# Performance work log

Measured on AMD Instinct MI355X. Metric: run time of the kernel, lower is better.

## Reference

```python
import jax, jax.numpy as jnp
import numpy as np

B, CIN, H, W = 32, 192, 56, 56
COUT, K, PAD, STRIDE = 192, 3, 1, 1


def setup_inputs() -> dict:
    key = jax.random.key(0)
    k1, k2 = jax.random.split(key, 2)
    x = jax.random.normal(k1, (B, CIN, H, W), dtype=jnp.float32)
    # torch Linear: weight [out_feature, in_feature*k*k], bias [out_feature]
    weight = jax.random.normal(k2, (COUT, CIN * K * K), dtype=jnp.float32) * 0.02
    bias = jnp.zeros((COUT,), dtype=jnp.float32)
    return {"x": x, "weight": weight, "bias": bias}


def reference(x, weight, bias):
    # pad H/W with zeros (F.pad constant)
    xp = jnp.pad(x, ((0, 0), (0, 0), (PAD, PAD), (PAD, PAD)))
    Bn, C, Hp, Wp = xp.shape
    Ho = (Hp - K) // STRIDE + 1
    Wo = (Wp - K) // STRIDE + 1
    # im2col matching torch.nn.Unfold layout: feature index = c*K*K + i*K + j
    # small fixed loop over K*K kernel offsets (9 slices), fully vectorized over B,C,Ho,Wo
    patches = jnp.stack(
        [xp[:, :, i : i + Ho * STRIDE : STRIDE, j : j + Wo * STRIDE : STRIDE]
         for i in range(K) for j in range(K)],
        axis=2,
    )  # [B, C, K*K, Ho, Wo]
    cols = patches.reshape(Bn, C * K * K, Ho * Wo)  # [B, C*K*K, L]
    # Linear over transposed unfold: out[b, l, o] = cols[b, :, l] @ weight[o, :].T + bias
    out = jnp.einsum('bkl,ok->bol', cols, weight) + bias[None, :, None]
    # rearrange 'b (h w) c -> b c h w' with h=w=sqrt(L)
    return out.reshape(Bn, COUT, Ho, Wo)
```

## Files before the change

### kernel.cpp

```cpp
#include <hip/hip_runtime.h>

typedef __attribute__((ext_vector_type(8))) short short8;
typedef __attribute__((ext_vector_type(4))) float floatx4;

#define CIN    192
#define COUTN  192
#define HWDIM  56
#define HWSZ   (56*56)
#define KWT    1728
#define TH     4
#define HY     6
#define PH     58
#define CK     32
#define NCHUNK 6
#define MT     64

#define XPACK_SHORTS (32u*6u*58u*58u*32u)
#define WPACK_SHORTS (3u*6u*9u*64u*32u)
#define WS_NEEDED    ((size_t)(XPACK_SHORTS + WPACK_SHORTS) * 2u)

__device__ __forceinline__ short f2bf(float f) {
    union { float f; unsigned u; } v; v.f = f;
    unsigned u = v.u + 0x7FFFu + ((v.u >> 16) & 1u);
    return (short)(u >> 16);
}

__global__ __launch_bounds__(256)
void pack_x(const float* __restrict__ x, short* __restrict__ xp) {
    int idx = blockIdx.x * 256 + threadIdx.x;
    const int TOT = 32 * 6 * 58 * 58 * 4;
    if (idx >= TOT) return;
    int cg  = idx & 3;
    int pix = idx >> 2;
    int xq  = pix % 58;
    int t   = pix / 58;
    int hq  = t % 58;
    int bc  = t / 58;
    int cc  = bc % 6;
    int b   = bc / 6;
    short8 v;
    if (hq == 0 || hq == 57 || xq == 0 || xq == 57) {
        v = (short8){0, 0, 0, 0, 0, 0, 0, 0};
    } else {
        const float* src = x + ((size_t)(b * CIN + cc * 32 + cg * 8) * HWDIM + (hq - 1)) * HWDIM + (xq - 1);
#pragma unroll
        for (int k = 0; k < 8; ++k) v[k] = f2bf(src[(size_t)k * HWSZ]);
    }
    *(short8*)(xp + (size_t)idx * 8) = v;
}

__global__ __launch_bounds__(256)
void pack_w(const float* __restrict__ w, short* __restrict__ wp) {
    int idx = blockIdx.x * 256 + threadIdx.x;
    const int TOT = 3 * 6 * 9 * 64 * 4;
    if (idx >= TOT) return;
    int cg = idx & 3;
    int m  = (idx >> 2) & 63;
    int t  = idx >> 8;
    int off = t % 9;  t /= 9;
    int cc  = t % 6;
    int og  = t / 6;
    short8 v;
#pragma unroll
    for (int k = 0; k < 8; ++k)
        v[k] = f2bf(w[(size_t)(og * 64 + m) * KWT + (cc * 32 + cg * 8 + k) * 9 + off]);
    *(short8*)(wp + (size_t)idx * 8) = v;
}

__global__ __launch_bounds__(256, 2)
void conv_main(const short* __restrict__ xp, const short* __restrict__ wp,
               const float* __restrict__ bias, float* __restrict__ out) {
    __shared__ __align__(16) short sh[HY * PH * CK];

    const int tid  = threadIdx.x;
    const int gh0  = blockIdx.x * TH;
    const int og   = blockIdx.y;
    const int bb   = blockIdx.z;
    const int lane = tid & 63;
    const int wave = tid >> 6;
    const int wm   = wave >> 1;
    const int wn   = wave & 1;
    const int g    = lane >> 4;
    const int col  = lane & 15;

    int ly[7], lx[7];
#pragma unroll
    for (int nt = 0; nt < 7; ++nt) {
        int l = wn * 112 + nt * 16 + col;
        ly[nt] = l / 56;
        lx[nt] = l % 56;
    }

    floatx4 acc[2][7];
#pragma unroll
    for (int mt = 0; mt < 2; ++mt)
#pragma unroll
        for (int nt = 0; nt < 7; ++nt)
            acc[mt][nt] = (floatx4){0.f, 0.f, 0.f, 0.f};

    const short8* wpk = (const short8*)wp;
    const int wlbase = wave * 64;

    for (int cc = 0; cc < NCHUNK; ++cc) {
        if (cc) __syncthreads();

        const short* src = xp + ((size_t)(bb * 6 + cc) * (PH * PH) + (size_t)gh0 * PH) * CK;
#pragma unroll
        for (int j = 0; j < 6; ++j) {
            int idx = j * 256 + tid;
            if (idx < HY * PH * 4) {
                __builtin_amdgcn_global_load_lds(
                    (const __attribute__((address_space(1))) void*)(src + (size_t)idx * 8),
                    (__attribute__((address_space(3))) void*)(sh + (j * 256 + wlbase) * 8),
                    16, 0, 0);
            }
        }

        short8 afr[9][2];
#pragma unroll
        for (int off = 0; off < 9; ++off)
#pragma unroll
            for (int mt = 0; mt < 2; ++mt)
                afr[off][mt] = wpk[((og * 6 + cc) * 9 + off) * 256 + (wm * 32 + mt * 16 + col) * 4 + g];

        __syncthreads();

#pragma unroll
        for (int off = 0; off < 9; ++off) {
            const int di = off / 3, dj = off % 3;
#pragma unroll
            for (int nt = 0; nt < 7; ++nt) {
                short8 bfr = *(const short8*)&sh[((ly[nt] + di) * PH + lx[nt] + dj) * CK + g * 8];
                acc[0][nt] = __builtin_amdgcn_mfma_f32_16x16x32_bf16(afr[off][0], bfr, acc[0][nt], 0, 0, 0);
                acc[1][nt] = __builtin_amdgcn_mfma_f32_16x16x32_bf16(afr[off][1], bfr, acc[1][nt], 0, 0, 0);
            }
        }
    }

#pragma unroll
    for (int mt = 0; mt < 2; ++mt) {
        int o = og * 64 + wm * 32 + mt * 16 + g * 4;
#pragma unroll
        for (int nt = 0; nt < 7; ++nt) {
            int l  = wn * 112 + nt * 16 + col;
            int h  = gh0 + l / 56;
            int ww = l % 56;
            size_t base = ((size_t)(bb * COUTN + o) * HWDIM + h) * HWDIM + ww;
            floatx4 v = acc[mt][nt];
#pragma unroll
            for (int r2 = 0; r2 < 4; ++r2)
                out[base + (size_t)r2 * HWSZ] = v[r2] + bias[o + r2];
        }
    }
}

__global__ __launch_bounds__(256, 2)
void conv3x3_fb(const float* __restrict__ x, const float* __restrict__ w,
                const float* __restrict__ bias, float* __restrict__ out) {
    __shared__ __align__(16) short sh_halo[HY * PH * CK];
    __shared__ __align__(16) short sh_w[9 * MT * CK];
    const int tid = threadIdx.x;
    const int gh0 = blockIdx.x * TH;
    const int o0  = blockIdx.y * MT;
    const int bb  = blockIdx.z;
    const int lane = tid & 63, wave = tid >> 6;
    const int wm = wave >> 1, wn = wave & 1;
    const int g = lane >> 4, col = lane & 15;
    int ly[7], lx[7];
#pragma unroll
    for (int nt = 0; nt < 7; ++nt) {
        int l = wn * 112 + nt * 16 + col;
        ly[nt] = l / 56; lx[nt] = l % 56;
    }
    floatx4 acc[2][7];
#pragma unroll
    for (int mt = 0; mt < 2; ++mt)
#pragma unroll
        for (int nt = 0; nt < 7; ++nt) acc[mt][nt] = (floatx4){0.f,0.f,0.f,0.f};
    for (int cc = 0; cc < NCHUNK; ++cc) {
        const int c0 = cc * CK;
        if (cc) __syncthreads();
        for (int i = tid; i < 4 * HY * PH; i += 256) {
            int xx = i % PH, r = i / PH, y = r % HY, cg = r / HY;
            int gh = gh0 + y - 1, gw = xx - 1;
            bool ok = ((unsigned)gh < 56u) & ((unsigned)gw < 56u);
            const float* src = x + ((size_t)(bb * CIN + c0 + cg * 8) * HWDIM + gh) * HWDIM + gw;
            short8 v;
#pragma unroll
            for (int k = 0; k < 8; ++k) v[k] = f2bf(ok ? src[k * HWSZ] : 0.f);
            *(short8*)&sh_halo[(y * PH + xx) * CK + ((cg ^ ((xx >> 1) & 3)) << 3)] = v;
        }
        for (int i = tid; i < 9 * MT * 4; i += 256) {
            int cg = i & 3, off = (i >> 2) % 9, m = i / 36;
            const float* src = w + (size_t)(o0 + m) * KWT + (c0 + cg * 8) * 9 + off;
            short8 v;
#pragma unroll
            for (int k = 0; k < 8; ++k) v[k] = f2bf(src[k * 9]);
            *(short8*)&sh_w[(off * MT + m) * CK + ((cg ^ ((m >> 1) & 3)) << 3)] = v;
        }
        __syncthreads();
#pragma unroll
        for (int off = 0; off < 9; ++off) {
            const int di = off / 3, dj = off % 3;
            short8 a[2];
#pragma unroll
            for (int mt = 0; mt < 2; ++mt) {
                int m = wm * 32 + mt * 16 + col;
                a[mt] = *(const short8*)&sh_w[(off * MT + m) * CK + ((g ^ ((m >> 1) & 3)) << 3)];
            }
#pragma unroll
            for (int nt = 0; nt < 7; ++nt) {
                int yy = ly[nt] + di, xpp = lx[nt] + dj;
                short8 bfr = *(const short8*)&sh_halo[(yy * PH + xpp) * CK + ((g ^ ((xpp >> 1) & 3)) << 3)];
                acc[0][nt] = __builtin_amdgcn_mfma_f32_16x16x32_bf16(a[0], bfr, acc[0][nt], 0, 0, 0);
                acc[1][nt] = __builtin_amdgcn_mfma_f32_16x16x32_bf16(a[1], bfr, acc[1][nt], 0, 0, 0);
            }
        }
    }
#pragma unroll
    for (int mt = 0; mt < 2; ++mt) {
        int o = o0 + wm * 32 + mt * 16 + g * 4;
#pragma unroll
        for (int nt = 0; nt < 7; ++nt) {
            int l = wn * 112 + nt * 16 + col;
            int h = gh0 + l / 56, ww = l % 56;
            size_t base = ((size_t)(bb * COUTN + o) * HWDIM + h) * HWDIM + ww;
            floatx4 v = acc[mt][nt];
#pragma unroll
            for (int r2 = 0; r2 < 4; ++r2)
                out[base + (size_t)r2 * HWSZ] = v[r2] + bias[o + r2];
        }
    }
}

extern "C" void kernel_launch(void* const* d_in, const int* in_sizes, int n_in,
                              void* d_out, int out_size, void* d_ws, size_t ws_size,
                              hipStream_t stream) {
    const float* x  = (const float*)d_in[0];
    const float* wt = (const float*)d_in[1];
    const float* bi = (const float*)d_in[2];
    float* out = (float*)d_out;

    if (ws_size >= WS_NEEDED) {
        short* xpk = (short*)d_ws;
        short* wpk = xpk + XPACK_SHORTS;
        {
            int tot = 32 * 6 * 58 * 58 * 4;
            pack_x<<<(tot + 255) / 256, 256, 0, stream>>>(x, xpk);
        }
        {
            int tot = 3 * 6 * 9 * 64 * 4;
            pack_w<<<(tot + 255) / 256, 256, 0, stream>>>(wt, wpk);
        }
        conv_main<<<dim3(14, 3, 32), dim3(256), 0, stream>>>(xpk, wpk, bi, out);
    } else {
        conv3x3_fb<<<dim3(14, 3, 32), dim3(256), 0, stream>>>(x, wt, bi, out);
    }
}
```

Before: 205.4 us.

## Enlarge conv tile to 8 rows, swizzle LDS halo, and coalesce x packing

The main conv kernel now covers 8 output rows per block instead of 4. Each wave handles all 64 output channels over 112 pixels, so the B fragments read from LDS are reused across four MFMA M-tiles, and weights are loaded per offset rather than all upfront. The halo is written to LDS with an XOR swizzle of channel groups to reduce bank conflicts. pack_x is rewritten to read x with coalesced float4 loads per row and transpose through LDS, which fixes the strided gather. The trade-off is more accumulator registers (4x7 floatx4) under launch bounds of 2 blocks per CU, a larger halo in LDS, and half as many blocks.

```diff
diff --git a/kernel.cpp b/kernel.cpp
--- a/kernel.cpp
+++ b/kernel.cpp
@@ -8,12 +8,9 @@
 #define HWDIM  56
 #define HWSZ   (56*56)
 #define KWT    1728
-#define TH     4
-#define HY     6
 #define PH     58
 #define CK     32
 #define NCHUNK 6
-#define MT     64
 
 #define XPACK_SHORTS (32u*6u*58u*58u*32u)
 #define WPACK_SHORTS (3u*6u*9u*64u*32u)
@@ -27,26 +24,39 @@
 
 __global__ __launch_bounds__(256)
 void pack_x(const float* __restrict__ x, short* __restrict__ xp) {
-    int idx = blockIdx.x * 256 + threadIdx.x;
-    const int TOT = 32 * 6 * 58 * 58 * 4;
-    if (idx >= TOT) return;
-    int cg  = idx & 3;
-    int pix = idx >> 2;
-    int xq  = pix % 58;
-    int t   = pix / 58;
-    int hq  = t % 58;
-    int bc  = t / 58;
-    int cc  = bc % 6;
-    int b   = bc / 6;
-    short8 v;
-    if (hq == 0 || hq == 57 || xq == 0 || xq == 57) {
-        v = (short8){0, 0, 0, 0, 0, 0, 0, 0};
-    } else {
-        const float* src = x + ((size_t)(b * CIN + cc * 32 + cg * 8) * HWDIM + (hq - 1)) * HWDIM + (xq - 1);
-#pragma unroll
-        for (int k = 0; k < 8; ++k) v[k] = f2bf(src[(size_t)k * HWSZ]);
-    }
-    *(short8*)(xp + (size_t)idx * 8) = v;
+    const int hq = blockIdx.x;
+    const int cc = blockIdx.y;
+    const int b  = blockIdx.z;
+    const int tid = threadIdx.x;
+    short* dst = xp + ((size_t)((b * 6 + cc) * 58 + hq) * 58) * CK;
+
+    if (hq == 0 || hq == 57) {
+        if (tid < 232) *(short8*)(dst + tid * 8) = (short8){0,0,0,0,0,0,0,0};
+        return;
+    }
+
+    __shared__ unsigned lds[56 * 20];
+    const int h = hq - 1;
+
+    if (tid < 224) {
+        int cpair = tid / 14, f4 = tid % 14;
+        const float* s1 = x + ((size_t)(b * CIN + cc * 32 + cpair * 2) * HWSZ) + h * 56 + f4 * 4;
+        floatx4 v1 = *(const floatx4*)s1;
+        floatx4 v2 = *(const floatx4*)(s1 + HWSZ);
+#pragma unroll
+        for (int k = 0; k < 4; ++k) {
+            unsigned pr = (unsigned short)f2bf(v1[k]) | ((unsigned)(unsigned short)f2bf(v2[k]) << 16);
+            lds[(f4 * 4 + k) * 20 + cpair] = pr;
+        }
+    }
+    __syncthreads();
+    if (tid < 232) {
+        int xq = tid >> 2, q = tid & 3;
+        short8 v = (short8){0,0,0,0,0,0,0,0};
+        if (xq >= 1 && xq <= 56)
+            v = *(const short8*)&lds[(xq - 1) * 20 + q * 4];
+        *(short8*)(dst + tid * 8) = v;
+    }
 }
 
 __global__ __launch_bounds__(256)
@@ -70,86 +80,87 @@
 __global__ __launch_bounds__(256, 2)
 void conv_main(const short* __restrict__ xp, const short* __restrict__ wp,
                const float* __restrict__ bias, float* __restrict__ out) {
-    __shared__ __align__(16) short sh[HY * PH * CK];
+    __shared__ __align__(16) short sh[10 * PH * CK];
 
     const int tid  = threadIdx.x;
-    const int gh0  = blockIdx.x * TH;
+    const int gh0  = blockIdx.x * 8;
     const int og   = blockIdx.y;
     const int bb   = blockIdx.z;
     const int lane = tid & 63;
     const int wave = tid >> 6;
-    const int wm   = wave >> 1;
-    const int wn   = wave & 1;
     const int g    = lane >> 4;
     const int col  = lane & 15;
 
-    int ly[7], lx[7];
+    int pb[7];
 #pragma unroll
     for (int nt = 0; nt < 7; ++nt) {
-        int l = wn * 112 + nt * 16 + col;
-        ly[nt] = l / 56;
-        lx[nt] = l % 56;
-    }
-
-    floatx4 acc[2][7];
-#pragma unroll
-    for (int mt = 0; mt < 2; ++mt)
+        int l = wave * 112 + nt * 16 + col;
+        pb[nt] = (l / 56) * PH + (l % 56);
+    }
+
+    floatx4 acc[4][7];
+#pragma unroll
+    for (int mt = 0; mt < 4; ++mt)
 #pragma unroll
         for (int nt = 0; nt < 7; ++nt)
             acc[mt][nt] = (floatx4){0.f, 0.f, 0.f, 0.f};
 
     const short8* wpk = (const short8*)wp;
-    const int wlbase = wave * 64;
 
     for (int cc = 0; cc < NCHUNK; ++cc) {
         if (cc) __syncthreads();
 
         const short* src = xp + ((size_t)(bb * 6 + cc) * (PH * PH) + (size_t)gh0 * PH) * CK;
 #pragma unroll
-        for (int j = 0; j < 6; ++j) {
+        for (int j = 0; j < 10; ++j) {
             int idx = j * 256 + tid;
-            if (idx < HY * PH * 4) {
+            if (idx < 2320) {
+                int p  = idx >> 2, sg = idx & 3;
+                int gc = (p << 2) | (sg ^ ((p >> 1) & 3));
                 __builtin_amdgcn_global_load_lds(
-                    (const __attribute__((address_space(1))) void*)(src + (size_t)idx * 8),
-                    (__attribute__((address_space(3))) void*)(sh + (j * 256 + wlbase) * 8),
+                    (const __attribute__((address_space(1))) void*)(src + (size_t)gc * 8),
+                    (__attribute__((address_space(3))) void*)(sh + (j * 256 + wave * 64) * 8),
                     16, 0, 0);
             }
         }
-
-        short8 afr[9][2];
-#pragma unroll
-        for (int off = 0; off < 9; ++off)
-#pragma unroll
-            for (int mt = 0; mt < 2; ++mt)
-                afr[off][mt] = wpk[((og * 6 + cc) * 9 + off) * 256 + (wm * 32 + mt * 16 + col) * 4 + g];
-
         __syncthreads();
 
+        const int wb = (og * 6 + cc) * 9 * 256;
 #pragma unroll
         for (int off = 0; off < 9; ++off) {
             const int di = off / 3, dj = off % 3;
+            short8 afr[4];
+#pragma unroll
+            for (int mt = 0; mt < 4; ++mt)
+                afr[mt] = wpk[wb + off * 256 + (mt * 16 + col) * 4 + g];
 #pragma unroll
             for (int nt = 0; nt < 7; ++nt) {
-                short8 bfr = *(const short8*)&sh[((ly[nt] + di) * PH + lx[nt] + dj) * CK + g * 8];
-                acc[0][nt] = __builtin_amdgcn_mfma_f32_16x16x32_bf16(afr[off][0], bfr, acc[0][nt], 0, 0, 0);
-                acc[1][nt] = __builtin_amdgcn_mfma_f32_16x16x32_bf16(afr[off][1], bfr, acc[1][nt], 0, 0, 0);
-            }
-        }
-    }
-
-#pragma unroll
-    for (int mt = 0; mt < 2; ++mt) {
-        int o = og * 64 + wm * 32 + mt * 16 + g * 4;
+                int p  = pb[nt] + di * PH + dj;
+                int ch = (p << 2) | (g ^ ((p >> 1) & 3));
+                short8 bfr = *(const short8*)&sh[ch * 8];
+                acc[0][nt] = __builtin_amdgcn_mfma_f32_16x16x32_bf16(afr[0], bfr, acc[0][nt], 0, 0, 0);
+                acc[1][nt] = __builtin_amdgcn_mfma_f32_16x16x32_bf16(afr[1], bfr, acc[1][nt], 0, 0, 0);
+                acc[2][nt] = __builtin_amdgcn_mfma_f32_16x16x32_bf16(afr[2], bfr, acc[2][nt], 0, 0, 0);
+                acc[3][nt] = __builtin_amdgcn_mfma_f32_16x16x32_bf16(afr[3], bfr, acc[3][nt], 0, 0, 0);
+            }
+        }
+    }
+
+#pragma unroll
+    for (int mt = 0; mt < 4; ++mt) {
+        int o = og * 64 + mt * 16 + g * 4;
+        float b0 = bias[o], b1 = bias[o + 1], b2 = bias[o + 2], b3 = bias[o + 3];
 #pragma unroll
         for (int nt = 0; nt < 7; ++nt) {
-            int l  = wn * 112 + nt * 16 + col;
+            int l  = wave * 112 + nt * 16 + col;
             int h  = gh0 + l / 56;
             int ww = l % 56;
             size_t base = ((size_t)(bb * COUTN + o) * HWDIM + h) * HWDIM + ww;
             floatx4 v = acc[mt][nt];
-#pragma unroll
-            for (int r2 = 0; r2 < 4; ++r2)
-                out[base + (size_t)r2 * HWSZ] = v[r2] + bias[o + r2];
+            out[base]                     = v[0] + b0;
+            out[base + (size_t)HWSZ]      = v[1] + b1;
+            out[base + (size_t)2 * HWSZ]  = v[2] + b2;
+            out[base + (size_t)3 * HWSZ]  = v[3] + b3;
         }
     }
 }
@@ -157,11 +168,11 @@
 __global__ __launch_bounds__(256, 2)
 void conv3x3_fb(const float* __restrict__ x, const float* __restrict__ w,
                 const float* __restrict__ bias, float* __restrict__ out) {
-    __shared__ __align__(16) short sh_halo[HY * PH * CK];
-    __shared__ __align__(16) short sh_w[9 * MT * CK];
+    __shared__ __align__(16) short sh_halo[6 * 58 * 32];
+    __shared__ __align__(16) short sh_w[9 * 64 * 32];
     const int tid = threadIdx.x;
-    const int gh0 = blockIdx.x * TH;
-    const int o0  = blockIdx.y * MT;
+    const int gh0 = blockIdx.x * 4;
+    const int o0  = blockIdx.y * 64;
     const int bb  = blockIdx.z;
     const int lane = tid & 63, wave = tid >> 6;
     const int wm = wave >> 1, wn = wave & 1;
@@ -178,25 +189,25 @@
 #pragma unroll
         for (int nt = 0; nt < 7; ++nt) acc[mt][nt] = (floatx4){0.f,0.f,0.f,0.f};
     for (int cc = 0; cc < NCHUNK; ++cc) {
-        const int c0 = cc * CK;
+        const int c0 = cc * 32;
         if (cc) __syncthreads();
-        for (int i = tid; i < 4 * HY * PH; i += 256) {
-            int xx = i % PH, r = i / PH, y = r % HY, cg = r / HY;
+        for (int i = tid; i < 4 * 6 * 58; i += 256) {
+            int xx = i % 58, r = i / 58, y = r % 6, cg = r / 6;
             int gh = gh0 + y - 1, gw = xx - 1;
             bool ok = ((unsigned)gh < 56u) & ((unsigned)gw < 56u);
             const float* src = x + ((size_t)(bb * CIN + c0 + cg * 8) * HWDIM + gh) * HWDIM + gw;
             short8 v;
 #pragma unroll
             for (int k = 0; k < 8; ++k) v[k] = f2bf(ok ? src[k * HWSZ] : 0.f);
-            *(short8*)&sh_halo[(y * PH + xx) * CK + ((cg ^ ((xx >> 1) & 3)) << 3)] = v;
-        }
-        for (int i = tid; i < 9 * MT * 4; i += 256) {
+            *(short8*)&sh_halo[(y * 58 + xx) * 32 + ((cg ^ ((xx >> 1) & 3)) << 3)] = v;
+        }
+        for (int i = tid; i < 9 * 64 * 4; i += 256) {
             int cg = i & 3, off = (i >> 2) % 9, m = i / 36;
             const float* src = w + (size_t)(o0 + m) * KWT + (c0 + cg * 8) * 9 + off;
             short8 v;
 #pragma unroll
             for (int k = 0; k < 8; ++k) v[k] = f2bf(src[k * 9]);
-            *(short8*)&sh_w[(off * MT + m) * CK + ((cg ^ ((m >> 1) & 3)) << 3)] = v;
+            *(short8*)&sh_w[(off * 64 + m) * 32 + ((cg ^ ((m >> 1) & 3)) << 3)] = v;
         }
         __syncthreads();
 #pragma unroll
@@ -206,12 +217,12 @@
 #pragma unroll
             for (int mt = 0; mt < 2; ++mt) {
                 int m = wm * 32 + mt * 16 + col;
-                a[mt] = *(const short8*)&sh_w[(off * MT + m) * CK + ((g ^ ((m >> 1) & 3)) << 3)];
+                a[mt] = *(const short8*)&sh_w[(off * 64 + m) * 32 + ((g ^ ((m >> 1) & 3)) << 3)];
             }
 #pragma unroll
             for (int nt = 0; nt < 7; ++nt) {
                 int yy = ly[nt] + di, xpp = lx[nt] + dj;
-                short8 bfr = *(const short8*)&sh_halo[(yy * PH + xpp) * CK + ((g ^ ((xpp >> 1) & 3)) << 3)];
+                short8 bfr = *(const short8*)&sh_halo[(yy * 58 + xpp) * 32 + ((g ^ ((xpp >> 1) & 3)) << 3)];
                 acc[0][nt] = __builtin_amdgcn_mfma_f32_16x16x32_bf16(a[0], bfr, acc[0][nt], 0, 0, 0);
                 acc[1][nt] = __builtin_amdgcn_mfma_f32_16x16x32_bf16(a[1], bfr, acc[1][nt], 0, 0, 0);
             }
@@ -244,15 +255,12 @@
     if (ws_size >= WS_NEEDED) {
         short* xpk = (short*)d_ws;
         short* wpk = xpk + XPACK_SHORTS;
-        {
-            int tot = 32 * 6 * 58 * 58 * 4;
-            pack_x<<<(tot + 255) / 256, 256, 0, stream>>>(x, xpk);
-        }
+        pack_x<<<dim3(58, 6, 32), 256, 0, stream>>>(x, xpk);
         {
             int tot = 3 * 6 * 9 * 64 * 4;
             pack_w<<<(tot + 255) / 256, 256, 0, stream>>>(wt, wpk);
         }
-        conv_main<<<dim3(14, 3, 32), dim3(256), 0, stream>>>(xpk, wpk, bi, out);
+        conv_main<<<dim3(7, 3, 32), dim3(256), 0, stream>>>(xpk, wpk, bi, out);
     } else {
         conv3x3_fb<<<dim3(14, 3, 32), dim3(256), 0, stream>>>(x, wt, bi, out);
     }
```

Measured after the change: 224.4 us. +9.3%, slower.
